# Kernel optimization log

Hardware: AMD Instinct MI355X
Metric: run time of the kernel (lower is better)

## Reference

```python
import jax, jax.numpy as jnp
import numpy as np

WIN = 7
SIZE = 56
HEADS = 16
DIM = 512
SHIFT = WIN // 2  # 3


def _rel_index():
    # Matches torch.meshgrid (ij) + flatten + pairwise diff indexing of the bias table.
    coords = np.stack(np.meshgrid(np.arange(WIN), np.arange(WIN), indexing='ij')).reshape(2, -1)  # [2,49]
    rel = (coords[:, :, None] - coords[:, None, :]).transpose(1, 2, 0)  # [49,49,2]
    rel[..., 0] += WIN - 1
    rel[..., 1] += WIN - 1
    rel[..., 0] *= 2 * WIN - 1
    return (rel[..., 0] + rel[..., 1]).reshape(-1)  # [49*49]


def _attn_mask():
    # Shifted-window mask: windows mixing different regions get -100 on cross pairs.
    img = np.zeros((SIZE, SIZE))
    sl = (slice(0, -WIN), slice(-WIN, -SHIFT), slice(-SHIFT, None))
    cnt = 0
    for h in sl:
        for w in sl:
            img[h, w] = cnt
            cnt += 1
    m = img.reshape(SIZE // WIN, WIN, SIZE // WIN, WIN).transpose(0, 2, 1, 3).reshape(-1, WIN * WIN)  # [nW,49]
    am = m[:, None, :] - m[:, :, None]  # [nW,49,49]
    return np.where(am != 0, -100.0, 0.0).astype(np.float32)


_REL_IDX = _rel_index()
_MASK = _attn_mask()  # [64,49,49]


def setup_inputs() -> dict:
    key = jax.random.key(0)
    ks = jax.random.split(key, 6)
    Bn, N, C = 2048, WIN * WIN, DIM
    return {
        'x': jax.random.normal(ks[0], (Bn, N, C), jnp.float32),
        'qkv_w': jax.random.normal(ks[1], (C, 3 * C), jnp.float32) * (C ** -0.5),
        'qkv_b': jax.random.normal(ks[2], (3 * C,), jnp.float32) * 0.02,
        'proj_w': jax.random.normal(ks[3], (C, C), jnp.float32) * (C ** -0.5),
        'proj_b': jax.random.normal(ks[4], (C,), jnp.float32) * 0.02,
        'bias_table': jax.random.normal(ks[5], ((2 * WIN - 1) ** 2, HEADS), jnp.float32) * 0.02,
    }


def reference(x, qkv_w, qkv_b, proj_w, proj_b, bias_table):
    Bn, N, C = x.shape
    D = C // HEADS
    qkv = (x @ qkv_w + qkv_b).reshape(Bn, N, 3, HEADS, D).transpose(2, 0, 3, 1, 4)  # [3,Bn,H,N,D]
    q, k, v = qkv[0] * (D ** -0.5), qkv[1], qkv[2]
    attn = jnp.einsum('bhnd,bhmd->bhnm', q, k)  # [Bn,H,N,N]
    bias = bias_table[jnp.asarray(_REL_IDX)].reshape(N, N, HEADS).transpose(2, 0, 1)  # [H,N,N]
    attn = attn + bias[None]
    mask = jnp.asarray(_MASK, x.dtype)  # [nW,N,N]
    nW = mask.shape[0]
    attn = attn.reshape(Bn // nW, nW, HEADS, N, N) + mask[None, :, None]
    attn = jax.nn.softmax(attn.reshape(Bn, HEADS, N, N), axis=-1)
    out = jnp.einsum('bhnm,bhmd->bhnd', attn, v).transpose(0, 2, 1, 3).reshape(Bn, N, C)
    return out @ proj_w + proj_b
```

## Files before the change

### kernel.cpp

```cpp
#include <hip/hip_runtime.h>
#include <hip/hip_bf16.h>
#include <stdint.h>


#define HEADS 16
#define NTOK  49
#define CH    512

typedef float  f32x4  __attribute__((ext_vector_type(4)));
typedef __bf16 bf16x8 __attribute__((ext_vector_type(8)));
typedef unsigned short u16;
typedef unsigned int   u32;

__device__ __forceinline__ u16 f2bf(float f) {
  return __builtin_bit_cast(u16, (__bf16)f);
}

__device__ __forceinline__ void gload16(const u16* g, u16* l) {
  __builtin_amdgcn_global_load_lds(
      (const __attribute__((address_space(1))) u32*)g,
      (__attribute__((address_space(3))) u32*)l, 16, 0, 0);
}

__global__ __launch_bounds__(256) void k_wprep(const float* __restrict__ qkv_w,
                                               const float* __restrict__ proj_w,
                                               u16* __restrict__ Wt, u16* __restrict__ Pt) {
  __shared__ float tile[32][33];
  const float sc = 0.17677669529663687f;
  int b = blockIdx.x;
  const float* src; u16* dst; int ld, tk, tn, scaleN;
  if (b < 768) { src = qkv_w; dst = Wt; ld = 1536; tk = (b / 48) * 32; tn = (b % 48) * 32; scaleN = 512; }
  else { b -= 768; src = proj_w; dst = Pt; ld = 512; tk = (b / 16) * 32; tn = (b % 16) * 32; scaleN = 0; }
  const int c = threadIdx.x & 31, r0 = threadIdx.x >> 5;
#pragma unroll
  for (int i = 0; i < 4; ++i) {
    int r = r0 + i * 8;
    tile[r][c] = src[(size_t)(tk + r) * ld + tn + c];
  }
  __syncthreads();
#pragma unroll
  for (int i = 0; i < 4; ++i) {
    int r = r0 + i * 8;
    float v = tile[c][r];
    if (tn + r < scaleN) v *= sc;
    dst[(size_t)(tn + r) * 512 + tk + c] = f2bf(v);
  }
}

__global__ __launch_bounds__(256) void k_xcast(const float* __restrict__ x,
                                               u16* __restrict__ xb) {
  int tid = blockIdx.x * 256 + threadIdx.x;
  const float4* xv = (const float4*)x;
  float4 a = xv[tid * 2], b = xv[tid * 2 + 1];
  u16 o[8] = {f2bf(a.x), f2bf(a.y), f2bf(a.z), f2bf(a.w),
              f2bf(b.x), f2bf(b.y), f2bf(b.z), f2bf(b.w)};
  ((int4*)xb)[tid] = *(const int4*)o;
}

__global__ __launch_bounds__(256) void k_tabs(const float* __restrict__ bias_table,
                                              const float* __restrict__ qkv_b,
                                              float* __restrict__ biasM,
                                              float* __restrict__ maskT,
                                              float* __restrict__ bias2) {
  const float sc = 0.17677669529663687f;
  int tid = blockIdx.x * 256 + threadIdx.x;
  if (tid < 1536) bias2[tid] = qkv_b[tid] * (tid < 512 ? sc : 1.f);
  if (tid < 16 * 4096) {
    int h = tid >> 12, rc = tid & 4095, r = rc >> 6, c = rc & 63;
    float v = -1e30f;
    if (r < NTOK && c < NTOK) {
      int ih = r / 7, iw = r - ih * 7, jh = c / 7, jw = c - jh * 7;
      v = bias_table[((ih - jh + 6) * 13 + (iw - jw + 6)) * HEADS + h];
    }
    biasM[tid] = v;
  } else {
    int t2 = tid - 65536;
    int mw = t2 >> 12, rc = t2 & 4095, r = rc >> 6, c = rc & 63;
    float v = 0.f;
    if (r < NTOK && c < NTOK) {
      int mwR = (mw >> 3) * 7, mwC = (mw & 7) * 7;
      int ih = r / 7, iw = r - ih * 7, jh = c / 7, jw = c - jh * 7;
      int gih = mwR + ih, giw = mwC + iw, gjh = mwR + jh, gjw = mwC + jw;
      int ri = (gih < 49 ? 0 : (gih < 53 ? 1 : 2)) * 3 + (giw < 49 ? 0 : (giw < 53 ? 1 : 2));
      int rj = (gjh < 49 ? 0 : (gjh < 53 ? 1 : 2)) * 3 + (gjw < 49 ? 0 : (gjw < 53 ? 1 : 2));
      v = (ri != rj) ? -100.f : 0.f;
    }
    maskT[t2] = v;
  }
}

template<int OUT_F32>
__global__ __launch_bounds__(256, 2) void k_gemm(const u16* __restrict__ A,
                                                 const u16* __restrict__ Bt,
                                                 const float* __restrict__ bias,
                                                 void* __restrict__ Cp,
                                                 int M, int Nn, int K, int nbn) {
  __shared__ u16 smem[2 * 16384];
  const int t   = threadIdx.x;
  const int q8  = gridDim.x >> 3;
  const int bid = (blockIdx.x & 7) * q8 + (blockIdx.x >> 3);
  const int cb  = bid % nbn, rb = bid / nbn;
  const int row0 = rb << 7, col0 = cb << 7;
  const int lane = t & 63, w = t >> 6;
  const int wr = (w >> 1) << 6, wc = (w & 1) << 6;
  const int lm = lane & 15, lk = lane >> 4;

  const f32x4 fz = {0.f, 0.f, 0.f, 0.f};
  f32x4 acc[4][4];
#pragma unroll
  for (int i = 0; i < 4; i++)
#pragma unroll
    for (int j = 0; j < 4; j++) acc[i][j] = fz;

  int gr[4], gc[4], gdb[4];
#pragma unroll
  for (int i = 0; i < 4; ++i) {
    int q = (i << 8) + t;
    gr[i]  = q >> 3;
    gc[i]  = (((q & 7) ^ (gr[i] & 7)) << 3);
    gdb[i] = ((i << 8) + (t & 192)) << 3;
  }
  int offA[4], offB[4];
#pragma unroll
  for (int i = 0; i < 4; ++i) {
    int rowA = wr + i * 16 + lm;
    offA[i] = rowA * 64 + ((lk ^ (rowA & 7)) << 3);
    int rowB = wc + i * 16 + lm;
    offB[i] = rowB * 64 + ((lk ^ (rowB & 7)) << 3);
  }

  auto stage = [&](int p, int kt) {
    const int kb = kt << 6;
    u16* dA = smem + p * 16384;
    u16* dB = dA + 8192;
#pragma unroll
    for (int i = 0; i < 4; ++i) {
      gload16(A  + (size_t)(row0 + gr[i]) * K + kb + gc[i], dA + gdb[i]);
      gload16(Bt + (size_t)(col0 + gr[i]) * K + kb + gc[i], dB + gdb[i]);
    }
  };

  const int nk = K >> 6;
  stage(0, 0);
  int p = 0;
  for (int kt = 0; kt < nk; ++kt) {
    if (kt + 1 < nk) {
      stage(p ^ 1, kt + 1);
      asm volatile("s_waitcnt vmcnt(8)" ::: "memory");
    } else {
      asm volatile("s_waitcnt vmcnt(0)" ::: "memory");
    }
    __builtin_amdgcn_s_barrier();
    asm volatile("" ::: "memory");
    const u16* sA = smem + p * 16384;
    const u16* sB = sA + 8192;
    bf16x8 a[4][2], b[4][2];
#pragma unroll
    for (int mi = 0; mi < 4; ++mi) {
      a[mi][0] = *(const bf16x8*)(sA + offA[mi]);
      a[mi][1] = *(const bf16x8*)(sA + (offA[mi] ^ 32));
    }
#pragma unroll
    for (int ni = 0; ni < 4; ++ni) {
      b[ni][0] = *(const bf16x8*)(sB + offB[ni]);
      b[ni][1] = *(const bf16x8*)(sB + (offB[ni] ^ 32));
    }
#pragma unroll
    for (int kk = 0; kk < 2; ++kk)
#pragma unroll
      for (int mi = 0; mi < 4; ++mi)
#pragma unroll
        for (int ni = 0; ni < 4; ++ni)
          acc[mi][ni] = __builtin_amdgcn_mfma_f32_16x16x32_bf16(a[mi][kk], b[ni][kk],
                                                                acc[mi][ni], 0, 0, 0);
    asm volatile("" ::: "memory");
    __builtin_amdgcn_s_barrier();
    asm volatile("" ::: "memory");
    p ^= 1;
  }

  if constexpr (!OUT_F32) {
#pragma unroll
    for (int mi = 0; mi < 4; ++mi)
#pragma unroll
      for (int ni = 0; ni < 4; ++ni) {
        int col = wc + ni * 16 + lm;
        float bv = bias[col0 + col];
#pragma unroll
        for (int r = 0; r < 4; ++r)
          smem[(wr + mi * 16 + lk * 4 + r) * 136 + col] = f2bf(acc[mi][ni][r] + bv);
      }
    __syncthreads();
    const int rr = t >> 1, seg = t & 1;
    u16* dst = (u16*)Cp + (size_t)(row0 + rr) * Nn + col0 + seg * 64;
    const u16* src = smem + rr * 136 + seg * 64;
#pragma unroll
    for (int i = 0; i < 8; ++i)
      *(int4*)(dst + i * 8) = *(const int4*)(src + i * 8);
  } else {
    float* smf = (float*)smem;
    for (int half = 0; half < 2; ++half) {
      __syncthreads();
      if ((w >> 1) == half) {
#pragma unroll
        for (int mi = 0; mi < 4; ++mi)
#pragma unroll
          for (int ni = 0; ni < 4; ++ni) {
            int col = wc + ni * 16 + lm;
            float bv = bias[col0 + col];
#pragma unroll
            for (int r = 0; r < 4; ++r)
              smf[(mi * 16 + lk * 4 + r) * 132 + col] = acc[mi][ni][r] + bv;
          }
      }
      __syncthreads();
      const int rr = t >> 2, seg = t & 3;
      float* dst = (float*)Cp + (size_t)(row0 + half * 64 + rr) * Nn + col0 + seg * 32;
      const float* src = smf + rr * 132 + seg * 32;
#pragma unroll
      for (int i = 0; i < 8; ++i)
        *(float4*)(dst + i * 4) = *(const float4*)(src + i * 4);
    }
  }
}

__global__ __launch_bounds__(256) void k_attn(const u16* __restrict__ qkv,
                                              const float* __restrict__ biasM,
                                              const float* __restrict__ maskT,
                                              u16* __restrict__ aout) {
  __shared__ u16 sm[4 * 3264];
  const int wdx = blockIdx.x;
  const int mw  = wdx & 63;
  const int t   = threadIdx.x;
  const int wv  = t >> 6;
  const int l   = t & 63;
  const int lm  = l & 15, lk = l >> 4;
  const size_t tb = (size_t)wdx * NTOK;
  const u16* base = qkv + tb * 1536;
  u16* sV = sm + wv * 3264;
  u16* sP = sV + 2176;

  const int4  iz = make_int4(0, 0, 0, 0);
  const f32x4 fz = {0.f, 0.f, 0.f, 0.f};
  const float* mT = maskT + (mw << 12);

  for (int hh = 0; hh < 4; ++hh) {
    const int h = (wv << 2) + hh;

    {
      int4 vv[4] = {iz, iz, iz, iz};
      if (l < NTOK) {
        const u16* vp = base + (size_t)l * 1536 + 1024 + h * 32;
#pragma unroll
        for (int i = 0; i < 4; ++i) vv[i] = *(const int4*)(vp + i * 8);
      }
      const u16* u = (const u16*)vv;
#pragma unroll
      for (int d = 0; d < 32; ++d) sV[d * 68 + l] = u[d];
    }

    bf16x8 kf[4];
#pragma unroll
    for (int ni = 0; ni < 4; ++ni) {
      int krow = ni * 16 + lm;
      int4 ki = (krow < NTOK)
        ? *(const int4*)(base + (size_t)krow * 1536 + 512 + h * 32 + lk * 8) : iz;
      kf[ni] = __builtin_bit_cast(bf16x8, ki);
    }

    bf16x8 vb[2][2];
#pragma unroll
    for (int kt = 0; kt < 2; ++kt)
#pragma unroll
      for (int df = 0; df < 2; ++df)
        vb[kt][df] = *(const bf16x8*)(sV + (df * 16 + lm) * 68 + kt * 32 + lk * 8);

    const float* bM = biasM + (h << 12);

#pragma unroll
    for (int mi = 0; mi < 4; ++mi) {
      const int qrow = mi * 16 + lm;
      int4 qi = (qrow < NTOK)
        ? *(const int4*)(base + (size_t)qrow * 1536 + h * 32 + lk * 8) : iz;
      bf16x8 qf = __builtin_bit_cast(bf16x8, qi);

      f32x4 st[4];
#pragma unroll
      for (int ni = 0; ni < 4; ++ni) {
        const int o4 = (qrow << 6) + ni * 16 + lk * 4;
        float4 b4 = *(const float4*)(bM + o4);
        float4 m4 = *(const float4*)(mT + o4);
        f32x4 ci = {b4.x + m4.x, b4.y + m4.y, b4.z + m4.z, b4.w + m4.w};
        st[ni] = __builtin_amdgcn_mfma_f32_16x16x32_bf16(kf[ni], qf, ci, 0, 0, 0);
      }

      float mx = -3e38f;
#pragma unroll
      for (int ni = 0; ni < 4; ++ni)
#pragma unroll
        for (int r = 0; r < 4; ++r) mx = fmaxf(mx, st[ni][r]);
      mx = fmaxf(mx, __shfl_xor(mx, 16, 64));
      mx = fmaxf(mx, __shfl_xor(mx, 32, 64));
      float sum = 0.f;
#pragma unroll
      for (int ni = 0; ni < 4; ++ni)
#pragma unroll
        for (int r = 0; r < 4; ++r) {
          float p = __expf(st[ni][r] - mx);
          st[ni][r] = p;
          sum += p;
        }
      sum += __shfl_xor(sum, 16, 64);
      sum += __shfl_xor(sum, 32, 64);
      const float rinv = __builtin_amdgcn_rcpf(sum);

#pragma unroll
      for (int ni = 0; ni < 4; ++ni) {
        u16 pk[4] = {f2bf(st[ni][0] * rinv), f2bf(st[ni][1] * rinv),
                     f2bf(st[ni][2] * rinv), f2bf(st[ni][3] * rinv)};
        *(int2*)(sP + lm * 68 + ni * 16 + lk * 4) = *(const int2*)pk;
      }

      f32x4 o0 = fz, o1 = fz;
#pragma unroll
      for (int kt = 0; kt < 2; ++kt) {
        bf16x8 pa = *(const bf16x8*)(sP + lm * 68 + kt * 32 + lk * 8);
        o0 = __builtin_amdgcn_mfma_f32_16x16x32_bf16(pa, vb[kt][0], o0, 0, 0, 0);
        o1 = __builtin_amdgcn_mfma_f32_16x16x32_bf16(pa, vb[kt][1], o1, 0, 0, 0);
      }

#pragma unroll
      for (int r = 0; r < 4; ++r) {
        int tok = mi * 16 + lk * 4 + r;
        if (tok < NTOK) {
          size_t ob = (tb + tok) * CH + h * 32;
          aout[ob + lm]      = f2bf(o0[r]);
          aout[ob + 16 + lm] = f2bf(o1[r]);
        }
      }
    }
  }
}

extern "C" void kernel_launch(void* const* d_in, const int* in_sizes, int n_in,
                              void* d_out, int out_size, void* d_ws, size_t ws_size,
                              hipStream_t stream) {
  const float* x      = (const float*)d_in[0];
  const float* qkv_b  = (const float*)d_in[2];
  const float* proj_b = (const float*)d_in[4];
  const float* btab   = (const float*)d_in[5];

  char* ws   = (char*)d_ws;
  u16* Wt    = (u16*)ws;
  u16* Pt    = (u16*)(ws + 1572864);
  u16* qkv   = (u16*)(ws + 2097152);
  u16* aout  = (u16*)(ws + 2097152 + 308281344ull);
  u16* xb    = aout;
  float* biasM = (float*)(ws + 2097152 + 308281344ull + 102760448ull);
  float* maskT = biasM + 65536;
  float* bias2 = maskT + 262144;
  float* out = (float*)d_out;

  k_wprep<<<1024, 256, 0, stream>>>((const float*)d_in[1], (const float*)d_in[3], Wt, Pt);
  k_xcast<<<25088, 256, 0, stream>>>(x, xb);
  k_tabs<<<1280, 256, 0, stream>>>(btab, qkv_b, biasM, maskT, bias2);
  k_gemm<0><<<784 * 12, 256, 0, stream>>>(xb, Wt, bias2, (void*)qkv, 100352, 1536, 512, 12);
  k_attn<<<2048, 256, 0, stream>>>(qkv, biasM, maskT, aout);
  k_gemm<1><<<784 * 4, 256, 0, stream>>>(aout, Pt, proj_b, (void*)out, 100352, 512, 512, 4);
}
```

Measured before the change: 598.2 us.

## Fuse fp32-to-bf16 input cast into QKV GEMM A-tile loading

Removes the separate x cast kernel and has the QKV GEMM load fp32 x tiles into registers, convert them to bf16 and write them into swizzled LDS. The B tiles still use direct global-to-LDS loads. This avoids writing and re-reading a bf16 copy of x and saves one launch. The cost is fp32 A traffic for every column block and register-staged loads instead of async LDS loads, which may lower GEMM efficiency.

```diff
diff --git a/kernel.cpp b/kernel.cpp
--- a/kernel.cpp
+++ b/kernel.cpp
@@ -45,16 +45,6 @@
     if (tn + r < scaleN) v *= sc;
     dst[(size_t)(tn + r) * 512 + tk + c] = f2bf(v);
   }
-}
-
-__global__ __launch_bounds__(256) void k_xcast(const float* __restrict__ x,
-                                               u16* __restrict__ xb) {
-  int tid = blockIdx.x * 256 + threadIdx.x;
-  const float4* xv = (const float4*)x;
-  float4 a = xv[tid * 2], b = xv[tid * 2 + 1];
-  u16 o[8] = {f2bf(a.x), f2bf(a.y), f2bf(a.z), f2bf(a.w),
-              f2bf(b.x), f2bf(b.y), f2bf(b.z), f2bf(b.w)};
-  ((int4*)xb)[tid] = *(const int4*)o;
 }
 
 __global__ __launch_bounds__(256) void k_tabs(const float* __restrict__ bias_table,
@@ -89,8 +79,8 @@
   }
 }
 
-template<int OUT_F32>
-__global__ __launch_bounds__(256, 2) void k_gemm(const u16* __restrict__ A,
+template<int A_F32, int OUT_F32>
+__global__ __launch_bounds__(256, 2) void k_gemm(const void* __restrict__ Ap,
                                                  const u16* __restrict__ Bt,
                                                  const float* __restrict__ bias,
                                                  void* __restrict__ Cp,
@@ -129,26 +119,65 @@
     offB[i] = rowB * 64 + ((lk ^ (rowB & 7)) << 3);
   }
 
-  auto stage = [&](int p, int kt) {
+  auto stageB = [&](int p, int kt) {
     const int kb = kt << 6;
+    u16* dB = smem + p * 16384 + 8192;
+#pragma unroll
+    for (int i = 0; i < 4; ++i)
+      gload16(Bt + (size_t)(col0 + gr[i]) * K + kb + gc[i], dB + gdb[i]);
+  };
+  auto stageA16 = [&](int p, int kt) {
+    const int kb = kt << 6;
+    const u16* A = (const u16*)Ap;
     u16* dA = smem + p * 16384;
-    u16* dB = dA + 8192;
-#pragma unroll
-    for (int i = 0; i < 4; ++i) {
-      gload16(A  + (size_t)(row0 + gr[i]) * K + kb + gc[i], dA + gdb[i]);
-      gload16(Bt + (size_t)(col0 + gr[i]) * K + kb + gc[i], dB + gdb[i]);
-    }
+#pragma unroll
+    for (int i = 0; i < 4; ++i)
+      gload16(A + (size_t)(row0 + gr[i]) * K + kb + gc[i], dA + gdb[i]);
   };
 
+  const int rAst = t >> 1, hA = t & 1;
+  float4 rf[8];
+  auto loadAf = [&](int kt) {
+    const float* xA = (const float*)Ap;
+    const int kb = kt << 6;
+    const float* src = xA + (size_t)(row0 + rAst) * K + kb + hA * 32;
+#pragma unroll
+    for (int i = 0; i < 8; ++i)
+      rf[i] = *(const float4*)(src + i * 4);
+  };
+  auto writeAf = [&](int p) {
+    u16* dA = smem + p * 16384;
+#pragma unroll
+    for (int j = 0; j < 4; ++j) {
+      u16 pk[8] = {f2bf(rf[2*j].x),   f2bf(rf[2*j].y),   f2bf(rf[2*j].z),   f2bf(rf[2*j].w),
+                   f2bf(rf[2*j+1].x), f2bf(rf[2*j+1].y), f2bf(rf[2*j+1].z), f2bf(rf[2*j+1].w)};
+      int sw = ((hA * 4 + j) ^ (rAst & 7)) << 3;
+      *(int4*)(dA + rAst * 64 + sw) = *(const int4*)pk;
+    }
+  };
+
   const int nk = K >> 6;
-  stage(0, 0);
+  if constexpr (A_F32) { loadAf(0); } else { stageA16(0, 0); }
+  stageB(0, 0);
   int p = 0;
   for (int kt = 0; kt < nk; ++kt) {
-    if (kt + 1 < nk) {
-      stage(p ^ 1, kt + 1);
-      asm volatile("s_waitcnt vmcnt(8)" ::: "memory");
+    if constexpr (A_F32) {
+      writeAf(p);
+      if (kt + 1 < nk) {
+        loadAf(kt + 1);
+        stageB(p ^ 1, kt + 1);
+        asm volatile("s_waitcnt vmcnt(12) lgkmcnt(0)" ::: "memory");
+      } else {
+        asm volatile("s_waitcnt vmcnt(0) lgkmcnt(0)" ::: "memory");
+      }
     } else {
-      asm volatile("s_waitcnt vmcnt(0)" ::: "memory");
+      if (kt + 1 < nk) {
+        stageA16(p ^ 1, kt + 1);
+        stageB(p ^ 1, kt + 1);
+        asm volatile("s_waitcnt vmcnt(8)" ::: "memory");
+      } else {
+        asm volatile("s_waitcnt vmcnt(0)" ::: "memory");
+      }
     }
     __builtin_amdgcn_s_barrier();
     asm volatile("" ::: "memory");
@@ -355,16 +384,16 @@
   u16* Pt    = (u16*)(ws + 1572864);
   u16* qkv   = (u16*)(ws + 2097152);
   u16* aout  = (u16*)(ws + 2097152 + 308281344ull);
-  u16* xb    = aout;
   float* biasM = (float*)(ws + 2097152 + 308281344ull + 102760448ull);
   float* maskT = biasM + 65536;
   float* bias2 = maskT + 262144;
   float* out = (float*)d_out;
 
   k_wprep<<<1024, 256, 0, stream>>>((const float*)d_in[1], (const float*)d_in[3], Wt, Pt);
-  k_xcast<<<25088, 256, 0, stream>>>(x, xb);
   k_tabs<<<1280, 256, 0, stream>>>(btab, qkv_b, biasM, maskT, bias2);
-  k_gemm<0><<<784 * 12, 256, 0, stream>>>(xb, Wt, bias2, (void*)qkv, 100352, 1536, 512, 12);
+  k_gemm<1, 0><<<784 * 12, 256, 0, stream>>>((const void*)x, Wt, bias2, (void*)qkv,
+                                             100352, 1536, 512, 12);
   k_attn<<<2048, 256, 0, stream>>>(qkv, biasM, maskT, aout);
-  k_gemm<1><<<784 * 4, 256, 0, stream>>>(aout, Pt, proj_b, (void*)out, 100352, 512, 512, 4);
-}
+  k_gemm<0, 1><<<784 * 4, 256, 0, stream>>>((const void*)aout, Pt, proj_b, (void*)out,
+                                            100352, 512, 512, 4);
+}
```

Result: slower. 763.9 us (+27.7%).
